# Kernel tuning notes

Measured on AMD Instinct MI355X. Metric: run time of the kernel, lower is better.

The kernel has to match this reference:

```python
import jax, jax.numpy as jnp
import numpy as np

N_NODES = 100000
N_EDGES = 1600000
IN_F = 32
OUT_F = 64
KERNEL_SIZE = (5, 5)
DIM = 2
K_TOTAL = int(np.prod(KERNEL_SIZE))
# degree-1 (linear) B-spline: 2**dim corner combinations per edge
_COMBO = np.stack(np.meshgrid(*([[0, 1]] * DIM), indexing='ij'), axis=-1).reshape(-1, DIM)  # [S, dim]
_STRIDES = np.array([int(np.prod(KERNEL_SIZE[d + 1:])) for d in range(DIM)])  # row-major strides


def spline_basis(pseudo):
    # pseudo: [E, dim] in [0, 1]; degree-1 open B-spline per dimension.
    ks = jnp.asarray(KERNEL_SIZE)
    v = pseudo * (ks - 1).astype(pseudo.dtype)                   # [E, dim]
    i0 = jnp.clip(jnp.floor(v).astype(jnp.int32), 0, ks - 2)     # [E, dim] left knot
    frac = v - i0.astype(pseudo.dtype)
    amounts = jnp.stack([1.0 - frac, frac], axis=-1)             # [E, dim, 2]
    idxs = jnp.stack([i0, i0 + 1], axis=-1)                      # [E, dim, 2]
    combo = jnp.asarray(_COMBO)                                  # [S, dim]
    d_ar = jnp.arange(DIM)
    basis = jnp.prod(amounts[:, d_ar, combo], axis=-1)           # [E, S] product of per-dim weights
    kidx = jnp.sum(idxs[:, d_ar, combo] * jnp.asarray(_STRIDES), axis=-1)  # [E, S] flat kernel bin
    return basis, kidx


def setup_inputs() -> dict:
    key = jax.random.key(0)
    k1, k2, k3, k4, k5 = jax.random.split(key, 5)
    features = jax.random.normal(k1, (N_NODES, IN_F), dtype=jnp.float32)
    pseudo = jax.random.uniform(k2, (N_EDGES, DIM), dtype=jnp.float32)
    edge_index = jax.random.randint(k3, (2, N_EDGES), 0, N_NODES)
    stdv = 1.0 / float(np.sqrt(IN_F * K_TOTAL))  # matches reset_parameters
    weight = jax.random.uniform(k4, KERNEL_SIZE + (IN_F, OUT_F), minval=-stdv, maxval=stdv, dtype=jnp.float32)
    bias = jax.random.uniform(k5, (OUT_F,), minval=-stdv, maxval=stdv, dtype=jnp.float32)
    return {"features": features, "pseudo": pseudo, "edge_index": edge_index, "weight": weight, "bias": bias}


def reference(features, pseudo, edge_index, weight, bias):
    row, col = edge_index[0], edge_index[1]
    basis, kidx = spline_basis(pseudo)             # [E, S], [E, S]
    x = features[col]                              # [E, in] gather source features
    w = weight.reshape(K_TOTAL, IN_F, OUT_F)
    S = basis.shape[1]
    # Accumulate basis-weighted source features into (dest node, kernel bin) buckets,
    # then apply the per-bin weight matrices once. Mathematically identical to
    # per-edge gather of W[kidx], matmul, and scatter-sum over rows.
    H = jnp.zeros((N_NODES * K_TOTAL, IN_F), dtype=features.dtype)
    for s in range(S):  # small fixed loop over 2**dim spline corners
        seg = row * K_TOTAL + kidx[:, s]
        H = H + jax.ops.segment_sum(basis[:, s, None] * x, seg, num_segments=N_NODES * K_TOTAL)
    out = jnp.einsum('nki,kio->no', H.reshape(N_NODES, K_TOTAL, IN_F), w)
    return out + bias
```

## Files before the change

kernel.cpp:

```cpp
#include <hip/hip_runtime.h>

#define N_NODES 100000
#define N_EDGES 1600000
#define IN_F 32
#define OUT_F 64
#define K_TOTAL 25
#define CAP 31
#define OVF_CAP 8192

#define WS_CNT    0
#define WS_OVFCNT 400000
#define WS_WT4    400064
#define WS_OVF    604864
#define WS_REC    735936
#define WS_NEED   (735936 + (size_t)N_NODES * CAP * 8)

typedef float v2f __attribute__((ext_vector_type(2)));


__global__ __launch_bounds__(256) void transpose_w4(const float* __restrict__ W,
                                                    float* __restrict__ WT4f) {
    int idx = blockIdx.x * 256 + threadIdx.x;
    int j = idx >> 6, o = idx & 63;
    WT4f[((j >> 2) * 64 + o) * 4 + (j & 3)] = W[idx];
}

__global__ __launch_bounds__(256) void fill_bucket(const int* __restrict__ ei,
                                                   const float* __restrict__ pseudo,
                                                   int* __restrict__ cnt,
                                                   uint2* __restrict__ recs,
                                                   uint4* __restrict__ ovf,
                                                   int* __restrict__ ovfcnt) {
    int e = blockIdx.x * 256 + threadIdx.x;
    int row = ei[e];
    int col = ei[N_EDGES + e];
    float2 p = ((const float2*)pseudo)[e];
    float v0 = p.x * 4.0f, v1 = p.y * 4.0f;
    int i0 = min((int)v0, 3);
    int i1 = min((int)v1, 3);
    float f0 = v0 - (float)i0;
    float f1 = v1 - (float)i1;
    unsigned u0 = (unsigned)(f0 * 65535.0f + 0.5f);
    unsigned u1 = (unsigned)(f1 * 65535.0f + 0.5f);
    unsigned rx = (unsigned)col | ((unsigned)(i0 * 5 + i1) << 20);
    unsigned ry = u0 | (u1 << 16);
    int pos = atomicAdd(&cnt[row], 1);
    if (pos < CAP) {
        recs[(size_t)row * CAP + pos] = (uint2){rx, ry};
    } else {
        int j = atomicAdd(ovfcnt, 1);
        if (j < OVF_CAP) ovf[j] = (uint4){(unsigned)row, rx, ry, 0u};
    }
}

__global__ __launch_bounds__(256, 3) void fused4(
        const float* __restrict__ x, const float* __restrict__ WT4f,
        const float* __restrict__ bias, const int* __restrict__ cnt,
        const uint2* __restrict__ recs, float* __restrict__ out) {
    __shared__ float Hs[16 * 800];
    const int t = threadIdx.x;

    float4* L4 = (float4*)Hs;
    for (int i = t; i < 3200; i += 256) L4[i] = make_float4(0.f, 0.f, 0.f, 0.f);
    __syncthreads();

    {
        const int nn = t >> 4;
        const int fp = t & 15;
        const int n = blockIdx.x * 16 + nn;
        const int num = min(cnt[n], CAP);
        float* __restrict__ hb = Hs + nn * 800 + 2 * fp;

        if (num > 0) {
            const uint2* __restrict__ rp = recs + (size_t)n * CAP;
            const int last = num - 1;
            uint2 r0 = rp[0];
            uint2 r1 = rp[min(1, last)];
            uint2 r2 = rp[min(2, last)];
            uint2 r3 = rp[min(3, last)];
            float2 xv0 = *(const float2*)(x + (size_t)(r0.x & 0xFFFFF) * IN_F + 2 * fp);
            float2 xv1 = *(const float2*)(x + (size_t)(r1.x & 0xFFFFF) * IN_F + 2 * fp);

            for (int i = 0; i < num; ++i) {
                uint2 r4 = rp[min(i + 4, last)];
                float2 xn = *(const float2*)(x + (size_t)(r2.x & 0xFFFFF) * IN_F + 2 * fp);

                float f0 = (float)(r0.y & 0xFFFF) * (1.0f / 65535.0f);
                float f1 = (float)(r0.y >> 16) * (1.0f / 65535.0f);
                float a0 = 1.0f - f0, a1 = 1.0f - f1;
                float b0 = a0 * a1, b1 = a0 * f1, b2 = f0 * a1, b3 = f0 * f1;
                float* __restrict__ p = hb + ((r0.x >> 20) << 5);

                float2 h;
                h = *(float2*)(p);       h.x += b0 * xv0.x; h.y += b0 * xv0.y; *(float2*)(p)       = h;
                h = *(float2*)(p + 32);  h.x += b1 * xv0.x; h.y += b1 * xv0.y; *(float2*)(p + 32)  = h;
                h = *(float2*)(p + 160); h.x += b2 * xv0.x; h.y += b2 * xv0.y; *(float2*)(p + 160) = h;
                h = *(float2*)(p + 192); h.x += b3 * xv0.x; h.y += b3 * xv0.y; *(float2*)(p + 192) = h;

                r0 = r1; r1 = r2; r2 = r3; r3 = r4;
                xv0 = xv1; xv1 = xn;
            }
        }
    }
    __syncthreads();

    {
        const int o = t & 63;
        const int wv = t >> 6;
        const float4* __restrict__ wt = ((const float4*)WT4f) + o;
        const float* __restrict__ h0 = Hs + (wv * 4) * 800;

        v2f acc[4][2];
#pragma unroll
        for (int nd = 0; nd < 4; ++nd) { acc[nd][0] = (v2f)0.0f; acc[nd][1] = (v2f)0.0f; }

        for (int jq = 0; jq < 200; ++jq) {
            float4 w4 = wt[jq * 64];
            v2f wa = {w4.x, w4.y}, wb = {w4.z, w4.w};
#pragma unroll
            for (int nd = 0; nd < 4; ++nd) {
                float4 h4 = *(const float4*)(h0 + nd * 800 + jq * 4);
                v2f ha = {h4.x, h4.y}, hb2 = {h4.z, h4.w};
                acc[nd][0] += ha * wa;
                acc[nd][1] += hb2 * wb;
            }
        }
        float bo = bias[o];
        float* __restrict__ op = out + ((size_t)blockIdx.x * 16 + wv * 4) * 64 + o;
#pragma unroll
        for (int nd = 0; nd < 4; ++nd) {
            op[nd * 64] = bo + acc[nd][0].x + acc[nd][0].y + acc[nd][1].x + acc[nd][1].y;
        }
    }
}

__global__ __launch_bounds__(256) void ovf_fix(const float* __restrict__ x,
                                               const float* __restrict__ W,
                                               const uint4* __restrict__ ovf,
                                               const int* __restrict__ ovfcnt,
                                               float* __restrict__ out) {
    const int lane = threadIdx.x & 63;
    const int wv = threadIdx.x >> 6;
    int m = min(*ovfcnt, OVF_CAP);
    for (int idx = wv; idx < m; idx += 4) {
        uint4 v = ovf[idx];
        int row = (int)v.x;
        int col = (int)(v.y & 0xFFFFF);
        int kbase = (int)(v.y >> 20);
        float f0 = (float)(v.z & 0xFFFF) * (1.0f / 65535.0f);
        float f1 = (float)(v.z >> 16) * (1.0f / 65535.0f);
        float a0 = 1.0f - f0, a1 = 1.0f - f1;
        float bb[4] = {a0 * a1, a0 * f1, f0 * a1, f0 * f1};
        const int dk[4] = {0, 1, 5, 6};
        float acc = 0.0f;
#pragma unroll
        for (int s = 0; s < 4; ++s) {
            const float* __restrict__ Wk = W + (size_t)(kbase + dk[s]) * (IN_F * OUT_F);
            float part = 0.0f;
            for (int i = 0; i < IN_F; ++i)
                part += x[(size_t)col * IN_F + i] * Wk[i * OUT_F + lane];
            acc += bb[s] * part;
        }
        atomicAdd(&out[(size_t)row * OUT_F + lane], acc);
    }
}


__device__ __forceinline__ void basis_from(float p0, float p1, float b[4], int k[4]) {
    float v0 = p0 * 4.0f, v1 = p1 * 4.0f;
    int i0 = min(max((int)floorf(v0), 0), 3);
    int i1 = min(max((int)floorf(v1), 0), 3);
    float f0 = v0 - (float)i0, f1 = v1 - (float)i1;
    float a00 = 1.0f - f0, a10 = 1.0f - f1;
    b[0] = a00 * a10; k[0] = i0 * 5 + i1;
    b[1] = a00 * f1;  k[1] = i0 * 5 + i1 + 1;
    b[2] = f0 * a10;  k[2] = (i0 + 1) * 5 + i1;
    b[3] = f0 * f1;   k[3] = (i0 + 1) * 5 + i1 + 1;
}

__global__ __launch_bounds__(256) void bias_init(const float* __restrict__ bias,
                                                 float* __restrict__ out) {
    int idx = blockIdx.x * 256 + threadIdx.x;
    if (idx < N_NODES * OUT_F) out[idx] = bias[idx & 63];
}

__global__ __launch_bounds__(256) void spline_direct(
        const float* __restrict__ x, const float* __restrict__ pseudo,
        const int* __restrict__ ei, const float* __restrict__ W,
        float* __restrict__ out) {
    int gtid = blockIdx.x * 256 + threadIdx.x;
    int e = gtid >> 6;
    int lane = threadIdx.x & 63;
    if (e >= N_EDGES) return;
    int row = ei[e];
    int col = ei[N_EDGES + e];
    float b[4]; int k[4];
    basis_from(pseudo[e * 2 + 0], pseudo[e * 2 + 1], b, k);
    float xv = x[col * IN_F + (lane & 31)];
    float acc = 0.0f;
#pragma unroll
    for (int s = 0; s < 4; ++s) {
        const float* __restrict__ Wk = W + k[s] * (IN_F * OUT_F);
        float part = 0.0f;
#pragma unroll
        for (int i = 0; i < IN_F; ++i) {
            float xi = __shfl(xv, i, 64);
            part += xi * Wk[i * OUT_F + lane];
        }
        acc += b[s] * part;
    }
    atomicAdd(&out[row * OUT_F + lane], acc);
}

extern "C" void kernel_launch(void* const* d_in, const int* in_sizes, int n_in,
                              void* d_out, int out_size, void* d_ws, size_t ws_size,
                              hipStream_t stream) {
    const float* features = (const float*)d_in[0];
    const float* pseudo   = (const float*)d_in[1];
    const int*   eidx     = (const int*)d_in[2];
    const float* weight   = (const float*)d_in[3];
    const float* bias     = (const float*)d_in[4];
    float* out = (float*)d_out;

    char* ws = (char*)d_ws;

    if (ws_size >= WS_NEED) {
        int*   cnt    = (int*)(ws + WS_CNT);
        int*   ovfcnt = (int*)(ws + WS_OVFCNT);
        float* WT4f   = (float*)(ws + WS_WT4);
        uint4* ovf    = (uint4*)(ws + WS_OVF);
        uint2* recs   = (uint2*)(ws + WS_REC);

        hipMemsetAsync(cnt, 0, 400016, stream);
        transpose_w4<<<200, 256, 0, stream>>>(weight, WT4f);
        fill_bucket<<<N_EDGES / 256, 256, 0, stream>>>(eidx, pseudo, cnt, recs, ovf, ovfcnt);
        fused4<<<N_NODES / 16, 256, 0, stream>>>(features, WT4f, bias, cnt, recs, out);
        ovf_fix<<<1, 256, 0, stream>>>(features, weight, ovf, ovfcnt, out);
    } else {
        int blocks = (N_NODES * OUT_F + 255) / 256;
        bias_init<<<blocks, 256, 0, stream>>>(bias, out);
        long long total = (long long)N_EDGES * 64;
        spline_direct<<<(int)((total + 255) / 256), 256, 0, stream>>>(
            features, pseudo, eidx, weight, out);
    }
}
```

Baseline: 448.0 us.

## Remap dense GEMM stage to split outputs across half-waves and process two edges per thread

```diff
diff --git a/kernel.cpp b/kernel.cpp
--- a/kernel.cpp
+++ b/kernel.cpp
@@ -10,7 +10,7 @@
 
 #define WS_CNT    0
 #define WS_OVFCNT 400000
-#define WS_WT4    400064
+#define WS_WQ     400064
 #define WS_OVF    604864
 #define WS_REC    735936
 #define WS_NEED   (735936 + (size_t)N_NODES * CAP * 8)
@@ -18,11 +18,14 @@
 typedef float v2f __attribute__((ext_vector_type(2)));
 
 
-__global__ __launch_bounds__(256) void transpose_w4(const float* __restrict__ W,
-                                                    float* __restrict__ WT4f) {
+__global__ __launch_bounds__(256) void pack_wq(const float* __restrict__ W,
+                                               float* __restrict__ WQ) {
     int idx = blockIdx.x * 256 + threadIdx.x;
-    int j = idx >> 6, o = idx & 63;
-    WT4f[((j >> 2) * 64 + o) * 4 + (j & 3)] = W[idx];
+    int j = idx >> 5, oo = idx & 31;
+    float w0 = W[j * 64 + oo];
+    float w1 = W[j * 64 + oo + 32];
+    int jq = j >> 2, jr = j & 3, jh = jr >> 1, jp = jr & 1;
+    ((float2*)WQ)[((jq * 2 + jh) * 32 + oo) * 2 + jp] = make_float2(w0, w1);
 }
 
 __global__ __launch_bounds__(256) void fill_bucket(const int* __restrict__ ei,
@@ -31,30 +34,34 @@
                                                    uint2* __restrict__ recs,
                                                    uint4* __restrict__ ovf,
                                                    int* __restrict__ ovfcnt) {
-    int e = blockIdx.x * 256 + threadIdx.x;
-    int row = ei[e];
-    int col = ei[N_EDGES + e];
-    float2 p = ((const float2*)pseudo)[e];
-    float v0 = p.x * 4.0f, v1 = p.y * 4.0f;
-    int i0 = min((int)v0, 3);
-    int i1 = min((int)v1, 3);
-    float f0 = v0 - (float)i0;
-    float f1 = v1 - (float)i1;
-    unsigned u0 = (unsigned)(f0 * 65535.0f + 0.5f);
-    unsigned u1 = (unsigned)(f1 * 65535.0f + 0.5f);
-    unsigned rx = (unsigned)col | ((unsigned)(i0 * 5 + i1) << 20);
-    unsigned ry = u0 | (u1 << 16);
-    int pos = atomicAdd(&cnt[row], 1);
-    if (pos < CAP) {
-        recs[(size_t)row * CAP + pos] = (uint2){rx, ry};
-    } else {
-        int j = atomicAdd(ovfcnt, 1);
-        if (j < OVF_CAP) ovf[j] = (uint4){(unsigned)row, rx, ry, 0u};
+    int base = blockIdx.x * 512 + threadIdx.x;
+#pragma unroll
+    for (int h = 0; h < 2; ++h) {
+        int e = base + h * 256;
+        int row = ei[e];
+        int col = ei[N_EDGES + e];
+        float2 p = ((const float2*)pseudo)[e];
+        float v0 = p.x * 4.0f, v1 = p.y * 4.0f;
+        int i0 = min((int)v0, 3);
+        int i1 = min((int)v1, 3);
+        float f0 = v0 - (float)i0;
+        float f1 = v1 - (float)i1;
+        unsigned u0 = (unsigned)(f0 * 65535.0f + 0.5f);
+        unsigned u1 = (unsigned)(f1 * 65535.0f + 0.5f);
+        unsigned rx = (unsigned)col | ((unsigned)(i0 * 5 + i1) << 20);
+        unsigned ry = u0 | (u1 << 16);
+        int pos = atomicAdd(&cnt[row], 1);
+        if (pos < CAP) {
+            recs[(size_t)row * CAP + pos] = (uint2){rx, ry};
+        } else {
+            int j = atomicAdd(ovfcnt, 1);
+            if (j < OVF_CAP) ovf[j] = (uint4){(unsigned)row, rx, ry, 0u};
+        }
     }
 }
 
 __global__ __launch_bounds__(256, 3) void fused4(
-        const float* __restrict__ x, const float* __restrict__ WT4f,
+        const float* __restrict__ x, const float* __restrict__ WQ,
         const float* __restrict__ bias, const int* __restrict__ cnt,
         const uint2* __restrict__ recs, float* __restrict__ out) {
     __shared__ float Hs[16 * 800];
@@ -105,32 +112,41 @@
     __syncthreads();
 
     {
-        const int o = t & 63;
+        const int lane = t & 63;
         const int wv = t >> 6;
-        const float4* __restrict__ wt = ((const float4*)WT4f) + o;
-        const float* __restrict__ h0 = Hs + (wv * 4) * 800;
-
-        v2f acc[4][2];
-#pragma unroll
-        for (int nd = 0; nd < 4; ++nd) { acc[nd][0] = (v2f)0.0f; acc[nd][1] = (v2f)0.0f; }
+        const int oo = lane & 31;
+        const int nh = lane >> 5;
+        const int nA = 4 * wv + nh;
+        const int nB = nA + 2;
+        const float* __restrict__ hA = Hs + nA * 800;
+        const float* __restrict__ hB = Hs + nB * 800;
+        const float4* __restrict__ wq = ((const float4*)WQ) + oo;
+
+        v2f accA0 = (v2f)0.0f, accA1 = (v2f)0.0f;
+        v2f accB0 = (v2f)0.0f, accB1 = (v2f)0.0f;
 
         for (int jq = 0; jq < 200; ++jq) {
-            float4 w4 = wt[jq * 64];
-            v2f wa = {w4.x, w4.y}, wb = {w4.z, w4.w};
-#pragma unroll
-            for (int nd = 0; nd < 4; ++nd) {
-                float4 h4 = *(const float4*)(h0 + nd * 800 + jq * 4);
-                v2f ha = {h4.x, h4.y}, hb2 = {h4.z, h4.w};
-                acc[nd][0] += ha * wa;
-                acc[nd][1] += hb2 * wb;
-            }
-        }
-        float bo = bias[o];
-        float* __restrict__ op = out + ((size_t)blockIdx.x * 16 + wv * 4) * 64 + o;
-#pragma unroll
-        for (int nd = 0; nd < 4; ++nd) {
-            op[nd * 64] = bo + acc[nd][0].x + acc[nd][0].y + acc[nd][1].x + acc[nd][1].y;
-        }
+            float4 w0 = wq[(jq * 2 + 0) * 32];
+            float4 w1 = wq[(jq * 2 + 1) * 32];
+            float4 a4 = *(const float4*)(hA + jq * 4);
+            float4 b4 = *(const float4*)(hB + jq * 4);
+
+            accA0 += (v2f){a4.x, a4.x} * (v2f){w0.x, w0.y};
+            accA1 += (v2f){a4.y, a4.y} * (v2f){w0.z, w0.w};
+            accA0 += (v2f){a4.z, a4.z} * (v2f){w1.x, w1.y};
+            accA1 += (v2f){a4.w, a4.w} * (v2f){w1.z, w1.w};
+            accB0 += (v2f){b4.x, b4.x} * (v2f){w0.x, w0.y};
+            accB1 += (v2f){b4.y, b4.y} * (v2f){w0.z, w0.w};
+            accB0 += (v2f){b4.z, b4.z} * (v2f){w1.x, w1.y};
+            accB1 += (v2f){b4.w, b4.w} * (v2f){w1.z, w1.w};
+        }
+        float bL = bias[oo];
+        float bH = bias[oo + 32];
+        float* __restrict__ outb = out + (size_t)blockIdx.x * 16 * 64;
+        outb[nA * 64 + oo]      = bL + accA0.x + accA1.x;
+        outb[nA * 64 + oo + 32] = bH + accA0.y + accA1.y;
+        outb[nB * 64 + oo]      = bL + accB0.x + accB1.x;
+        outb[nB * 64 + oo + 32] = bH + accB0.y + accB1.y;
     }
 }
 
@@ -227,14 +243,14 @@
     if (ws_size >= WS_NEED) {
         int*   cnt    = (int*)(ws + WS_CNT);
         int*   ovfcnt = (int*)(ws + WS_OVFCNT);
-        float* WT4f   = (float*)(ws + WS_WT4);
+        float* WQ     = (float*)(ws + WS_WQ);
         uint4* ovf    = (uint4*)(ws + WS_OVF);
         uint2* recs   = (uint2*)(ws + WS_REC);
 
         hipMemsetAsync(cnt, 0, 400016, stream);
-        transpose_w4<<<200, 256, 0, stream>>>(weight, WT4f);
-        fill_bucket<<<N_EDGES / 256, 256, 0, stream>>>(eidx, pseudo, cnt, recs, ovf, ovfcnt);
-        fused4<<<N_NODES / 16, 256, 0, stream>>>(features, WT4f, bias, cnt, recs, out);
+        pack_wq<<<100, 256, 0, stream>>>(weight, WQ);
+        fill_bucket<<<N_EDGES / 512, 256, 0, stream>>>(eidx, pseudo, cnt, recs, ovf, ovfcnt);
+        fused4<<<N_NODES / 16, 256, 0, stream>>>(features, WQ, bias, cnt, recs, out);
         ovf_fix<<<1, 256, 0, stream>>>(features, weight, ovf, ovfcnt, out);
     } else {
         int blocks = (N_NODES * OUT_F + 255) / 256;
```

Result: slower. 552.2 us (+23.2%).
